# Kernel tuning notes

Hardware: AMD Instinct MI355X
Metric: run time of the kernel (lower is better)

## Reference

```python
import jax, jax.numpy as jnp
import numpy as np

SR = 24000          # sampling_rate
MAX_H = 60          # min(n_harmonics=100, 60)


def _interp_linear(x, T):
    """Linear upsample along axis 1, align_corners=True. x: [B, C, F] -> [B, T, F]."""
    B, C, F = x.shape
    src = jnp.arange(T, dtype=x.dtype) * ((C - 1) / (T - 1))
    i0 = jnp.clip(jnp.floor(src).astype(jnp.int32), 0, C - 2)
    frac = (src - i0.astype(x.dtype))[None, :, None]
    return x[:, i0, :] * (1.0 - frac) + x[:, i0 + 1, :] * frac


def setup_inputs() -> dict:
    key = jax.random.key(0)
    k1, k2, k3, k4, k5 = jax.random.split(key, 5)
    B, T, H, C, NF = 8, 48000, MAX_H, 100, 5
    f0 = 100.0 + 300.0 * jax.random.uniform(k1, (B, T, 1), dtype=jnp.float32)
    amplitudes = jax.random.uniform(k2, (B, T, H), dtype=jnp.float32)
    formant_freqs = 200.0 + 3300.0 * jax.random.uniform(k3, (B, C, NF), dtype=jnp.float32)
    formant_bws = 50.0 + 150.0 * jax.random.uniform(k4, (B, C, NF), dtype=jnp.float32)
    formant_amps = jax.random.uniform(k5, (B, C, NF), dtype=jnp.float32)
    initial_phase = jnp.zeros((B, 1, 1), dtype=jnp.float32)
    return {"f0": f0, "amplitudes": amplitudes, "formant_freqs": formant_freqs,
            "formant_bws": formant_bws, "formant_amps": formant_amps,
            "initial_phase": initial_phase}


def reference(f0, amplitudes, formant_freqs, formant_bws, formant_amps, initial_phase):
    B, T, _ = f0.shape
    f0 = jax.lax.stop_gradient(f0)                    # torch: f0.detach()
    voiced = (f0[..., 0] > 0).astype(f0.dtype)        # [B, T]
    phase = jnp.cumsum(2.0 * np.pi * f0 / SR, axis=1) + initial_phase  # [B, T, 1]

    ff = _interp_linear(formant_freqs, T)             # [B, T, NF]
    fb = _interp_linear(formant_bws, T)
    fa = _interp_linear(formant_amps, T)

    h = jnp.arange(1, MAX_H + 1, dtype=f0.dtype)      # [H]
    h_freq = f0 * h                                   # [B, T, H]
    nyq = (h_freq < SR / 2).astype(f0.dtype)          # [B, T, H]

    # formant resonance factor: prod over formants of (1 + amp*bw^2/((h_freq-freq)^2+bw^2))
    factor = jnp.ones_like(h_freq)
    for f in range(ff.shape[-1]):                     # NF = 5, small fixed loop
        freq = ff[:, :, f:f + 1]
        bw = fb[:, :, f:f + 1]
        amp = fa[:, :, f:f + 1]
        factor = factor * (1.0 + amp * bw * bw / ((h_freq - freq) ** 2 + bw * bw))

    osc = jnp.sin(phase * h)                          # [B, T, H]
    signal = jnp.sum(osc * amplitudes * factor * nyq, axis=-1) * voiced  # [B, T]

    final_phase = jax.lax.stop_gradient(phase[:, -1:, :] % (2.0 * np.pi))  # [B, 1, 1]
    return signal, final_phase
```

## Files before the change

kernel.cpp:

```cpp
#include <hip/hip_runtime.h>
#include <math.h>

#define SRATE   24000.0
#define NB      8
#define NT      48000
#define NH      60
#define NC      100
#define NFMT    5
#define CTS     64
#define NCH     (NT / CTS)
#define NPAIR   (NCH / 2)
#define TWO_PI  6.283185307179586476925286766559
#define PSC     (1.0f / 1024.0f)
#define NYQS    11.71875f

typedef float v2f __attribute__((ext_vector_type(2)));

__global__ __launch_bounds__(256) void k_partial(const float* __restrict__ f0,
                                                 double* __restrict__ part) {
    int b = blockIdx.y;
    int ch = blockIdx.x * 4 + (threadIdx.x >> 6);
    int lane = threadIdx.x & 63;
    if (ch < NCH) {
        int t = ch * CTS + lane;
        double q = (double)f0[b * NT + t];
        #pragma unroll
        for (int off = 32; off > 0; off >>= 1)
            q += __shfl_down(q, off, 64);
        if (lane == 0) part[b * NCH + ch] = q;
    }
}

__global__ __launch_bounds__(256) void k_main(const float* __restrict__ f0,
                                              const float* __restrict__ amps,
                                              const float* __restrict__ ffq,
                                              const float* __restrict__ fbw,
                                              const float* __restrict__ fam,
                                              const float* __restrict__ initp,
                                              const double* __restrict__ part,
                                              float* __restrict__ out) {
    int b = blockIdx.y;
    int cp = blockIdx.x * 4 + (threadIdx.x >> 6);
    int lane = threadIdx.x & 63;
    if (cp >= NPAIR) return;
    int ch0 = cp * 2;
    int t0 = cp * 128;
    int g0 = lane >> 2, j = lane & 3;
    const float4 f4z = make_float4(0.f, 0.f, 0.f, 0.f);

    const float* ab = amps + (size_t)b * NT * NH;

    #define AMPLD(S0, S1, S2, S3, p)                                          \
        { const float4* rr =                                                  \
              (const float4*)(ab + (size_t)(t0 + (p) * 16 + g0) * NH);        \
          S0 = rr[j]; S1 = rr[4 + j]; S2 = rr[8 + j];                         \
          S3 = (j < 3) ? rr[12 + j] : f4z; }

    float4 A0, A1, A2, A3, B0, B1, B2, B3;
    AMPLD(A0, A1, A2, A3, 0)
    AMPLD(B0, B1, B2, B3, 1)

    const double* pb = part + b * NCH;
    double sl = 0.0;
    #pragma unroll
    for (int k = 0; k < 12; ++k) {
        int idx = k * 64 + lane;
        double v = (idx < NCH) ? pb[idx] : 0.0;
        if (idx < ch0) sl += v;
    }
    #pragma unroll
    for (int off = 1; off < 64; off <<= 1)
        sl += __shfl_xor(sl, off, 64);

    double initrev = (double)initp[b] * (1.0 / TWO_PI);

    if (cp == 0) {
        double sa = 0.0;
        #pragma unroll
        for (int k = 0; k < 12; ++k) {
            int idx = k * 64 + lane;
            if (idx < NCH) sa += pb[idx];
        }
        #pragma unroll
        for (int off = 1; off < 64; off <<= 1)
            sa += __shfl_xor(sa, off, 64);
        if (lane == 0) {
            double rv = sa * (1.0 / SRATE) + initrev;
            out[NB * NT + b] = (float)((rv - floor(rv)) * TWO_PI);
        }
    }

    float revA, f0sA, revB, f0sB;
    float fqA[NFMT], c1A[NFMT], c2A[NFMT], fqB[NFMT], c1B[NFMT], c2B[NFMT];

    auto chunk_pre = [&](int tl, double prefd, float& rev_o, float& f0s_o,
                         float (&fqo)[NFMT], float (&c1o)[NFMT],
                         float (&c2o)[NFMT]) -> double {
        float f0v = f0[b * NT + tl];
        double inc = (double)f0v;
        #pragma unroll
        for (int off = 1; off < 64; off <<= 1) {
            double n = __shfl_up(inc, off, 64);
            if (lane >= off) inc += n;
        }
        double rev = (prefd + inc) * (1.0 / SRATE) + initrev;
        rev_o = (float)(rev - floor(rev));
        f0s_o = f0v * PSC;
        double srcd = (double)tl * (99.0 / 47999.0);
        int i0 = (int)srcd;
        if (i0 > NC - 2) i0 = NC - 2;
        float frac = (float)(srcd - (double)i0);
        float omf = 1.0f - frac;
        const float* Fq = ffq + (b * NC + i0) * NFMT;
        const float* Bw = fbw + (b * NC + i0) * NFMT;
        const float* Am = fam + (b * NC + i0) * NFMT;
        #pragma unroll
        for (int f = 0; f < NFMT; ++f) {
            float fqv = Fq[f] * omf + Fq[NFMT + f] * frac;
            float bwv = Bw[f] * omf + Bw[NFMT + f] * frac;
            float amv = Am[f] * omf + Am[NFMT + f] * frac;
            float bws = bwv * PSC;
            fqo[f] = fqv * PSC;
            c2o[f] = bws * bws;
            c1o[f] = amv * c2o[f];
        }
        return __shfl(inc, 63, 64);
    };

    double tot0 = chunk_pre(t0 + lane, sl, revA, f0sA, fqA, c1A, c2A);
    chunk_pre(t0 + 64 + lane, sl + tot0, revB, f0sB, fqB, c1B, c2B);

    auto do_pass = [&](int p, float revLane, float f0sLane,
                       const float (&fqL)[NFMT], const float (&c1L)[NFMT],
                       const float (&c2L)[NFMT],
                       float4 q0, float4 q1, float4 q2, float4 q3) {
        int gp = ((p & 3) << 4) + g0;
        float f0s   = __shfl(f0sLane, gp, 64);
        float rev_g = __shfl(revLane, gp, 64);
        float fq[NFMT], c1[NFMT], c2[NFMT];
        #pragma unroll
        for (int f = 0; f < NFMT; ++f) {
            fq[f] = __shfl(fqL[f], gp, 64);
            c1[f] = __shfl(c1L[f], gp, 64);
            c2[f] = __shfl(c2L[f], gp, 64);
        }
        float hb = (float)(j << 2);
        auto sd = [&](float k) {
            return __builtin_amdgcn_sinf(
                __builtin_amdgcn_fractf((hb + k) * rev_g));
        };
        v2f s01 = {sd(1.0f),  sd(2.0f)};
        v2f s23 = {sd(3.0f),  sd(4.0f)};
        v2f s45 = {sd(17.0f), sd(18.0f)};
        v2f s67 = {sd(19.0f), sd(20.0f)};
        float c16 = __builtin_amdgcn_cosf(
            __builtin_amdgcn_fractf(16.0f * rev_g));
        v2f cv = {2.0f * c16, 2.0f * c16};
        v2f s89 = cv * s45 - s01;
        v2f sAB = cv * s67 - s23;
        v2f sCD = cv * s89 - s45;
        v2f sEF = cv * sAB - s67;
        v2f acc2 = {0.0f, 0.0f};
        auto pairf = [&](float h1, v2f sn, float a0, float a1) {
            v2f hfl = {h1, h1 + 1.0f};
            v2f hs = f0s * hfl;
            v2f pN = {1.0f, 1.0f}, pD = {1.0f, 1.0f};
            #pragma unroll
            for (int f = 0; f < NFMT; ++f) {
                v2f d = hs - fq[f];
                v2f e = d * d + c2[f];
                pN *= e + c1[f];
                pD *= e;
            }
            float R = __builtin_amdgcn_rcpf(pD.x * pD.y);
            v2f fac = {pN.x * pD.y * R, pN.y * pD.x * R};
            v2f fm;
            fm.x = (hs.x < NYQS) ? fac.x : 0.0f;
            fm.y = (hs.y < NYQS) ? fac.y : 0.0f;
            v2f aa = {a0, a1};
            acc2 += (sn * aa) * fm;
        };
        pairf(hb + 1.0f,  s01, q0.x, q0.y);
        pairf(hb + 3.0f,  s23, q0.z, q0.w);
        pairf(hb + 17.0f, s45, q1.x, q1.y);
        pairf(hb + 19.0f, s67, q1.z, q1.w);
        pairf(hb + 33.0f, s89, q2.x, q2.y);
        pairf(hb + 35.0f, sAB, q2.z, q2.w);
        pairf(hb + 49.0f, sCD, q3.x, q3.y);
        pairf(hb + 51.0f, sEF, q3.z, q3.w);
        float acc = acc2.x + acc2.y;
        acc += __shfl_xor(acc, 1, 64);
        acc += __shfl_xor(acc, 2, 64);
        if (j == 0) {
            if (!(f0s > 0.0f)) acc = 0.0f;
            out[b * NT + t0 + (p << 4) + g0] = acc;
        }
    };

    #pragma unroll 1
    for (int pg = 0; pg < 8; pg += 2) {
        bool cB = pg >= 4;
        float revL = cB ? revB : revA;
        float f0sL = cB ? f0sB : f0sA;
        float fqL[NFMT], c1L[NFMT], c2L[NFMT];
        #pragma unroll
        for (int f = 0; f < NFMT; ++f) {
            fqL[f] = cB ? fqB[f] : fqA[f];
            c1L[f] = cB ? c1B[f] : c1A[f];
            c2L[f] = cB ? c2B[f] : c2A[f];
        }
        do_pass(pg, revL, f0sL, fqL, c1L, c2L, A0, A1, A2, A3);
        if (pg < 6) {
            AMPLD(A0, A1, A2, A3, pg + 2)
        }
        do_pass(pg + 1, revL, f0sL, fqL, c1L, c2L, B0, B1, B2, B3);
        if (pg < 6) {
            AMPLD(B0, B1, B2, B3, pg + 3)
        }
    }
    #undef AMPLD
}

extern "C" void kernel_launch(void* const* d_in, const int* in_sizes, int n_in,
                              void* d_out, int out_size, void* d_ws, size_t ws_size,
                              hipStream_t stream) {
    const float* f0    = (const float*)d_in[0];
    const float* amps  = (const float*)d_in[1];
    const float* ffq   = (const float*)d_in[2];
    const float* fbw   = (const float*)d_in[3];
    const float* fam   = (const float*)d_in[4];
    const float* initp = (const float*)d_in[5];
    float* out = (float*)d_out;

    double* part = (double*)d_ws;

    dim3 gpart((NCH + 3) / 4, NB);
    k_partial<<<gpart, 256, 0, stream>>>(f0, part);
    dim3 gmain((NPAIR + 3) / 4, NB);
    k_main<<<gmain, 256, 0, stream>>>(f0, amps, ffq, fbw, fam, initp, part, out);
}
```

Before: 33.45 us.

## Process one 64-sample chunk per wavefront with float in-chunk scan and occupancy hint

Each wavefront now handles a single 64-sample chunk instead of a pair, which doubles the wavefront count and removes the chunk-A/B select logic and the loop. The in-chunk prefix scan of f0 now runs in float, added to a double-reduced fractional chunk offset, instead of a full double scan. __launch_bounds__(256,4) is added to cap register usage for higher occupancy. The cost is that the per-wave prologue (prefix sum over partials, formant interpolation) is repeated twice as often, and float phase accumulation slightly reduces precision.

```diff
diff --git a/kernel.cpp b/kernel.cpp
--- a/kernel.cpp
+++ b/kernel.cpp
@@ -9,7 +9,6 @@
 #define NFMT    5
 #define CTS     64
 #define NCH     (NT / CTS)
-#define NPAIR   (NCH / 2)
 #define TWO_PI  6.283185307179586476925286766559
 #define PSC     (1.0f / 1024.0f)
 #define NYQS    11.71875f
@@ -31,23 +30,21 @@
     }
 }
 
-__global__ __launch_bounds__(256) void k_main(const float* __restrict__ f0,
-                                              const float* __restrict__ amps,
-                                              const float* __restrict__ ffq,
-                                              const float* __restrict__ fbw,
-                                              const float* __restrict__ fam,
-                                              const float* __restrict__ initp,
-                                              const double* __restrict__ part,
-                                              float* __restrict__ out) {
+__global__ __launch_bounds__(256, 4) void k_main(const float* __restrict__ f0,
+                                                 const float* __restrict__ amps,
+                                                 const float* __restrict__ ffq,
+                                                 const float* __restrict__ fbw,
+                                                 const float* __restrict__ fam,
+                                                 const float* __restrict__ initp,
+                                                 const double* __restrict__ part,
+                                                 float* __restrict__ out) {
     int b = blockIdx.y;
-    int cp = blockIdx.x * 4 + (threadIdx.x >> 6);
+    int ch = blockIdx.x * 4 + (threadIdx.x >> 6);
     int lane = threadIdx.x & 63;
-    if (cp >= NPAIR) return;
-    int ch0 = cp * 2;
-    int t0 = cp * 128;
+    if (ch >= NCH) return;
+    int t0 = ch * CTS;
     int g0 = lane >> 2, j = lane & 3;
     const float4 f4z = make_float4(0.f, 0.f, 0.f, 0.f);
-
     const float* ab = amps + (size_t)b * NT * NH;
 
     #define AMPLD(S0, S1, S2, S3, p)                                          \
@@ -66,7 +63,7 @@
     for (int k = 0; k < 12; ++k) {
         int idx = k * 64 + lane;
         double v = (idx < NCH) ? pb[idx] : 0.0;
-        if (idx < ch0) sl += v;
+        if (idx < ch) sl += v;
     }
     #pragma unroll
     for (int off = 1; off < 64; off <<= 1)
@@ -74,7 +71,7 @@
 
     double initrev = (double)initp[b] * (1.0 / TWO_PI);
 
-    if (cp == 0) {
+    if (ch == 0) {
         double sa = 0.0;
         #pragma unroll
         for (int k = 0; k < 12; ++k) {
@@ -90,59 +87,49 @@
         }
     }
 
-    float revA, f0sA, revB, f0sB;
-    float fqA[NFMT], c1A[NFMT], c2A[NFMT], fqB[NFMT], c1B[NFMT], c2B[NFMT];
-
-    auto chunk_pre = [&](int tl, double prefd, float& rev_o, float& f0s_o,
-                         float (&fqo)[NFMT], float (&c1o)[NFMT],
-                         float (&c2o)[NFMT]) -> double {
-        float f0v = f0[b * NT + tl];
-        double inc = (double)f0v;
-        #pragma unroll
-        for (int off = 1; off < 64; off <<= 1) {
-            double n = __shfl_up(inc, off, 64);
-            if (lane >= off) inc += n;
-        }
-        double rev = (prefd + inc) * (1.0 / SRATE) + initrev;
-        rev_o = (float)(rev - floor(rev));
-        f0s_o = f0v * PSC;
-        double srcd = (double)tl * (99.0 / 47999.0);
-        int i0 = (int)srcd;
-        if (i0 > NC - 2) i0 = NC - 2;
-        float frac = (float)(srcd - (double)i0);
-        float omf = 1.0f - frac;
-        const float* Fq = ffq + (b * NC + i0) * NFMT;
-        const float* Bw = fbw + (b * NC + i0) * NFMT;
-        const float* Am = fam + (b * NC + i0) * NFMT;
+    double pfrac = sl * (1.0 / SRATE) + initrev;
+    float prefF = (float)(pfrac - floor(pfrac));
+
+    float f0v = f0[b * NT + t0 + lane];
+    float incf = f0v;
+    #pragma unroll
+    for (int off = 1; off < 64; off <<= 1) {
+        float n = __shfl_up(incf, off, 64);
+        if (lane >= off) incf += n;
+    }
+    float rev_l = __builtin_amdgcn_fractf(prefF + incf * (1.0f / 24000.0f));
+    float f0s_l = f0v * PSC;
+
+    double srcd = (double)(t0 + lane) * (99.0 / 47999.0);
+    int i0 = (int)srcd;
+    if (i0 > NC - 2) i0 = NC - 2;
+    float frac = (float)(srcd - (double)i0);
+    float omf = 1.0f - frac;
+    const float* Fq = ffq + (b * NC + i0) * NFMT;
+    const float* Bw = fbw + (b * NC + i0) * NFMT;
+    const float* Am = fam + (b * NC + i0) * NFMT;
+    float fqs[NFMT], c1s[NFMT], c2s[NFMT];
+    #pragma unroll
+    for (int f = 0; f < NFMT; ++f) {
+        float fqv = Fq[f] * omf + Fq[NFMT + f] * frac;
+        float bwv = Bw[f] * omf + Bw[NFMT + f] * frac;
+        float amv = Am[f] * omf + Am[NFMT + f] * frac;
+        float bws = bwv * PSC;
+        fqs[f] = fqv * PSC;
+        c2s[f] = bws * bws;
+        c1s[f] = amv * c2s[f];
+    }
+
+    auto do_pass = [&](int p, float4 q0, float4 q1, float4 q2, float4 q3) {
+        int gp = (p << 4) + g0;
+        float f0s   = __shfl(f0s_l, gp, 64);
+        float rev_g = __shfl(rev_l, gp, 64);
+        float fq[NFMT], c1[NFMT], c2[NFMT];
         #pragma unroll
         for (int f = 0; f < NFMT; ++f) {
-            float fqv = Fq[f] * omf + Fq[NFMT + f] * frac;
-            float bwv = Bw[f] * omf + Bw[NFMT + f] * frac;
-            float amv = Am[f] * omf + Am[NFMT + f] * frac;
-            float bws = bwv * PSC;
-            fqo[f] = fqv * PSC;
-            c2o[f] = bws * bws;
-            c1o[f] = amv * c2o[f];
-        }
-        return __shfl(inc, 63, 64);
-    };
-
-    double tot0 = chunk_pre(t0 + lane, sl, revA, f0sA, fqA, c1A, c2A);
-    chunk_pre(t0 + 64 + lane, sl + tot0, revB, f0sB, fqB, c1B, c2B);
-
-    auto do_pass = [&](int p, float revLane, float f0sLane,
-                       const float (&fqL)[NFMT], const float (&c1L)[NFMT],
-                       const float (&c2L)[NFMT],
-                       float4 q0, float4 q1, float4 q2, float4 q3) {
-        int gp = ((p & 3) << 4) + g0;
-        float f0s   = __shfl(f0sLane, gp, 64);
-        float rev_g = __shfl(revLane, gp, 64);
-        float fq[NFMT], c1[NFMT], c2[NFMT];
-        #pragma unroll
-        for (int f = 0; f < NFMT; ++f) {
-            fq[f] = __shfl(fqL[f], gp, 64);
-            c1[f] = __shfl(c1L[f], gp, 64);
-            c2[f] = __shfl(c2L[f], gp, 64);
+            fq[f] = __shfl(fqs[f], gp, 64);
+            c1[f] = __shfl(c1s[f], gp, 64);
+            c2[f] = __shfl(c2s[f], gp, 64);
         }
         float hb = (float)(j << 2);
         auto sd = [&](float k) {
@@ -197,27 +184,12 @@
         }
     };
 
-    #pragma unroll 1
-    for (int pg = 0; pg < 8; pg += 2) {
-        bool cB = pg >= 4;
-        float revL = cB ? revB : revA;
-        float f0sL = cB ? f0sB : f0sA;
-        float fqL[NFMT], c1L[NFMT], c2L[NFMT];
-        #pragma unroll
-        for (int f = 0; f < NFMT; ++f) {
-            fqL[f] = cB ? fqB[f] : fqA[f];
-            c1L[f] = cB ? c1B[f] : c1A[f];
-            c2L[f] = cB ? c2B[f] : c2A[f];
-        }
-        do_pass(pg, revL, f0sL, fqL, c1L, c2L, A0, A1, A2, A3);
-        if (pg < 6) {
-            AMPLD(A0, A1, A2, A3, pg + 2)
-        }
-        do_pass(pg + 1, revL, f0sL, fqL, c1L, c2L, B0, B1, B2, B3);
-        if (pg < 6) {
-            AMPLD(B0, B1, B2, B3, pg + 3)
-        }
-    }
+    do_pass(0, A0, A1, A2, A3);
+    AMPLD(A0, A1, A2, A3, 2)
+    do_pass(1, B0, B1, B2, B3);
+    AMPLD(B0, B1, B2, B3, 3)
+    do_pass(2, A0, A1, A2, A3);
+    do_pass(3, B0, B1, B2, B3);
     #undef AMPLD
 }
 
@@ -234,8 +206,7 @@
 
     double* part = (double*)d_ws;
 
-    dim3 gpart((NCH + 3) / 4, NB);
-    k_partial<<<gpart, 256, 0, stream>>>(f0, part);
-    dim3 gmain((NPAIR + 3) / 4, NB);
-    k_main<<<gmain, 256, 0, stream>>>(f0, amps, ffq, fbw, fam, initp, part, out);
+    dim3 gchunk((NCH + 3) / 4, NB);
+    k_partial<<<gchunk, 256, 0, stream>>>(f0, part);
+    k_main<<<gchunk, 256, 0, stream>>>(f0, amps, ffq, fbw, fam, initp, part, out);
 }
```

New measurement: 33.06 us. Within noise of the previous version (-1.2%).
